# Kernel tuning notes

Hardware: AMD Instinct MI355X
Metric: run time of the kernel (lower is better)

Reference implementation:

```python
import jax, jax.numpy as jnp
import numpy as np
import math

D_MODEL = 1024
NUM_HEADS = 16
D_K = D_MODEL // NUM_HEADS
SEQ = 4096
THETA = 10000.0


def _rope_tables(d_k, max_seq_len, theta):
    freqs = 1.0 / theta ** (jnp.arange(0, d_k, 2, dtype=jnp.float32) / d_k)  # (d_k/2,)
    pos = jnp.arange(max_seq_len, dtype=jnp.float32)
    ang = pos[:, None] * freqs[None, :]  # (S, d_k/2)
    return jnp.cos(ang), jnp.sin(ang)


def setup_inputs() -> dict:
    key = jax.random.key(0)
    ks = jax.random.split(key, 5)
    std = math.sqrt(2.0 / (D_MODEL + D_MODEL))
    def trunc_w(k):
        return jax.random.truncated_normal(k, -3.0, 3.0, (D_MODEL, D_MODEL), jnp.float32) * std
    x = jax.random.normal(ks[0], (1, SEQ, D_MODEL), jnp.float32)
    Wq, Wk, Wv, Wo = trunc_w(ks[1]), trunc_w(ks[2]), trunc_w(ks[3]), trunc_w(ks[4])
    cos, sin = _rope_tables(D_K, SEQ, THETA)
    positions = jnp.arange(SEQ, dtype=jnp.int32)
    return {"x": x, "Wq": Wq, "Wk": Wk, "Wv": Wv, "Wo": Wo,
            "cos": cos, "sin": sin, "positions": positions}


def _apply_rope(t, cos, sin, positions):
    # t: (b, h, s, d_k); cos/sin: (max_s, d_k/2)
    c = cos[positions][None, None]  # (1,1,s,d_k/2)
    s = sin[positions][None, None]
    x1, x2 = t[..., ::2], t[..., 1::2]
    rotated = jnp.stack([x1 * c - x2 * s, x1 * s + x2 * c], axis=-1)  # (b,h,s,d_k/2,2)
    return rotated.reshape(t.shape)


def reference(x, Wq, Wk, Wv, Wo, cos, sin, positions):
    b, s, d = x.shape
    h, dk = NUM_HEADS, D_K
    def proj(W):
        y = jnp.einsum('bsi,oi->bso', x, W)
        return y.reshape(b, s, h, dk).transpose(0, 2, 1, 3)  # (b,h,s,dk)
    Q, K, V = proj(Wq), proj(Wk), proj(Wv)
    Q = _apply_rope(Q, cos, sin, positions)
    K = _apply_rope(K, cos, sin, positions)
    scores = jnp.einsum('bhqd,bhkd->bhqk', Q, K) / math.sqrt(dk)
    causal = jnp.tril(jnp.ones((s, s), dtype=bool))
    scores = jnp.where(causal[None, None], scores, -jnp.inf)
    weights = jax.nn.softmax(scores, axis=-1)
    y = jnp.einsum('bhqk,bhkd->bhqd', weights, V)
    y = y.transpose(0, 2, 1, 3).reshape(b, s, d)
    return jnp.einsum('bsi,oi->bso', y, Wo)
```

## Files before the change

kernel.cpp:

```cpp
#include <hip/hip_runtime.h>
#include <math.h>

#define SEQ 4096
#define DM  1024
#define NH  16
#define DK  64

typedef __attribute__((ext_vector_type(4))) float f32x4;
typedef __attribute__((ext_vector_type(8))) short bf16x8;
typedef __attribute__((ext_vector_type(8))) unsigned short u16x8;

union FragU { u16x8 u; bf16x8 b; ushort4 q[2]; unsigned w[4]; };

__device__ __forceinline__ unsigned cvtpk(float a, float b) {
    unsigned r; asm("v_cvt_pk_bf16_f32 %0, %1, %2" : "=v"(r) : "v"(a), "v"(b)); return r;
}
__device__ __forceinline__ float fexp2(float x) {
    float r; asm("v_exp_f32 %0, %1" : "=v"(r) : "v"(x)); return r;
}
__device__ __forceinline__ float bf_f(unsigned short s) {
    return __uint_as_float(((unsigned)s) << 16);
}
__device__ __forceinline__ void split4(float4 v, ushort4& hv, ushort4& lv) {
    union { ushort4 q; unsigned w[2]; } H, L;
    H.w[0] = cvtpk(v.x, v.y); H.w[1] = cvtpk(v.z, v.w);
    const float rx = v.x - __uint_as_float(H.w[0] << 16);
    const float ry = v.y - __uint_as_float(H.w[0] & 0xffff0000u);
    const float rz = v.z - __uint_as_float(H.w[1] << 16);
    const float rw = v.w - __uint_as_float(H.w[1] & 0xffff0000u);
    L.w[0] = cvtpk(rx, ry); L.w[1] = cvtpk(rz, rw);
    hv = H.q; lv = L.q;
}
__device__ __forceinline__ void split1(float f, unsigned short& h, unsigned short& l) {
    const unsigned hw = cvtpk(f, f) & 0xffffu;
    h = (unsigned short)hw;
    const float r = f - __uint_as_float(hw << 16);
    l = (unsigned short)(__float_as_uint(r) >> 16);
}

template<int MODE>
__global__ __launch_bounds__(256, 2)
void gemm_mfma(const float* __restrict__ Af,
               const unsigned short* __restrict__ Ahi, const unsigned short* __restrict__ Alo,
               const float* __restrict__ W0, const float* __restrict__ W1,
               const float* __restrict__ W2,
               unsigned short* __restrict__ OQh, unsigned short* __restrict__ OQl,
               unsigned short* __restrict__ OKh, unsigned short* __restrict__ OKl,
               unsigned short* __restrict__ OVh,
               float* __restrict__ Ofp,
               const float* __restrict__ cosT, const float* __restrict__ sinT,
               const int* __restrict__ positions)
{
    constexpr int NT = (MODE == 4) ? 24 : 8;
    __shared__ unsigned short As[128][76];
    __shared__ unsigned short Bs[128][76];

    const int t   = threadIdx.x;
    const int bid = blockIdx.x;
    const int qpx = (32 * NT) >> 3;
    const int swz = (bid & 7) * qpx + (bid >> 3);
    const int by  = swz / NT;
    const int bxf = swz % NT;
    const int wt  = (MODE == 4) ? (bxf >> 3) : 0;
    const int bx  = (MODE == 4) ? (bxf & 7) : bxf;
    const int m0  = by * 128;
    const float* W = (MODE == 4) ? (wt == 0 ? W0 : (wt == 1 ? W1 : W2)) : W0;

    const int lane = t & 63, w = t >> 6;
    const int wr = w >> 1, wc = w & 1;
    const int l15 = lane & 15, lg = lane >> 4;

    const int ar = t >> 1, ah = t & 1;
    const float* Ap = (MODE == 4) ? &Af[(size_t)(m0 + ar) * DM + ah * 16] : nullptr;
    const unsigned short* Aph = (MODE == 0) ? &Ahi[(size_t)(m0 + ar) * DM + ah * 16] : nullptr;
    const unsigned short* Apl = (MODE == 0) ? &Alo[(size_t)(m0 + ar) * DM + ah * 16] : nullptr;
    const float* Wp = &W[(size_t)(bx * 128 + ar) * DM + ah * 16];

    f32x4 acc[4][4];
#pragma unroll
    for (int mi = 0; mi < 4; ++mi)
#pragma unroll
        for (int ni = 0; ni < 4; ++ni) acc[mi][ni] = (f32x4){0.f, 0.f, 0.f, 0.f};

    float4 pa[4], pb[4];
    u16x8 pah[2], pal[2];
    if constexpr (MODE == 4) {
#pragma unroll
        for (int g = 0; g < 4; ++g) pa[g] = *reinterpret_cast<const float4*>(Ap + g * 4);
    } else {
        pah[0] = *reinterpret_cast<const u16x8*>(Aph);
        pah[1] = *reinterpret_cast<const u16x8*>(Aph + 8);
        pal[0] = *reinterpret_cast<const u16x8*>(Apl);
        pal[1] = *reinterpret_cast<const u16x8*>(Apl + 8);
    }
#pragma unroll
    for (int g = 0; g < 4; ++g) pb[g] = *reinterpret_cast<const float4*>(Wp + g * 4);

    for (int kt = 0; kt < 32; ++kt) {
        if constexpr (MODE == 4) {
#pragma unroll
            for (int g = 0; g < 4; ++g) {
                ushort4 hv, lv;
                split4(pa[g], hv, lv);
                *reinterpret_cast<ushort4*>(&As[ar][8 * g + 4 * ah])      = hv;
                *reinterpret_cast<ushort4*>(&As[ar][32 + 8 * g + 4 * ah]) = lv;
            }
        } else {
            FragU h0, h1, l0, l1;
            h0.u = pah[0]; h1.u = pah[1]; l0.u = pal[0]; l1.u = pal[1];
            *reinterpret_cast<ushort4*>(&As[ar][0  + 4 * ah]) = h0.q[0];
            *reinterpret_cast<ushort4*>(&As[ar][8  + 4 * ah]) = h0.q[1];
            *reinterpret_cast<ushort4*>(&As[ar][16 + 4 * ah]) = h1.q[0];
            *reinterpret_cast<ushort4*>(&As[ar][24 + 4 * ah]) = h1.q[1];
            *reinterpret_cast<ushort4*>(&As[ar][32 + 4 * ah]) = l0.q[0];
            *reinterpret_cast<ushort4*>(&As[ar][40 + 4 * ah]) = l0.q[1];
            *reinterpret_cast<ushort4*>(&As[ar][48 + 4 * ah]) = l1.q[0];
            *reinterpret_cast<ushort4*>(&As[ar][56 + 4 * ah]) = l1.q[1];
        }
#pragma unroll
        for (int g = 0; g < 4; ++g) {
            ushort4 hv, lv;
            split4(pb[g], hv, lv);
            *reinterpret_cast<ushort4*>(&Bs[ar][8 * g + 4 * ah])      = hv;
            *reinterpret_cast<ushort4*>(&Bs[ar][32 + 8 * g + 4 * ah]) = lv;
        }
        __syncthreads();

        if (kt < 31) {
            const int ko = (kt + 1) * 32;
            if constexpr (MODE == 4) {
#pragma unroll
                for (int g = 0; g < 4; ++g)
                    pa[g] = *reinterpret_cast<const float4*>(Ap + ko + g * 4);
            } else {
                pah[0] = *reinterpret_cast<const u16x8*>(Aph + ko);
                pah[1] = *reinterpret_cast<const u16x8*>(Aph + ko + 8);
                pal[0] = *reinterpret_cast<const u16x8*>(Apl + ko);
                pal[1] = *reinterpret_cast<const u16x8*>(Apl + ko + 8);
            }
#pragma unroll
            for (int g = 0; g < 4; ++g)
                pb[g] = *reinterpret_cast<const float4*>(Wp + ko + g * 4);
        }

        FragU b_h[4], b_l[4];
#pragma unroll
        for (int ni = 0; ni < 4; ++ni) {
            const int row = wc * 64 + ni * 16 + l15;
            b_h[ni].u = *reinterpret_cast<const u16x8*>(&Bs[row][8 * lg]);
            b_l[ni].u = *reinterpret_cast<const u16x8*>(&Bs[row][32 + 8 * lg]);
        }
#pragma unroll
        for (int mi = 0; mi < 4; ++mi) {
            FragU a_h, a_l;
            const int row = wr * 64 + mi * 16 + l15;
            a_h.u = *reinterpret_cast<const u16x8*>(&As[row][8 * lg]);
            a_l.u = *reinterpret_cast<const u16x8*>(&As[row][32 + 8 * lg]);
#pragma unroll
            for (int ni = 0; ni < 4; ++ni) {
                f32x4 c = acc[mi][ni];
                c = __builtin_amdgcn_mfma_f32_16x16x32_bf16(a_h.b, b_h[ni].b, c, 0, 0, 0);
                c = __builtin_amdgcn_mfma_f32_16x16x32_bf16(a_h.b, b_l[ni].b, c, 0, 0, 0);
                c = __builtin_amdgcn_mfma_f32_16x16x32_bf16(a_l.b, b_h[ni].b, c, 0, 0, 0);
                acc[mi][ni] = c;
            }
        }
        __syncthreads();
    }

    if constexpr (MODE == 0) {
#pragma unroll
        for (int mi = 0; mi < 4; ++mi)
#pragma unroll
            for (int ni = 0; ni < 4; ++ni)
#pragma unroll
                for (int r = 0; r < 4; ++r) {
                    const int m = m0 + wr * 64 + mi * 16 + lg * 4 + r;
                    const int n = bx * 128 + wc * 64 + ni * 16 + l15;
                    Ofp[(size_t)m * DM + n] = acc[mi][ni][r];
                }
    } else if (wt == 2) {
#pragma unroll
        for (int mi = 0; mi < 4; ++mi)
#pragma unroll
            for (int ni = 0; ni < 4; ++ni) {
                ushort4 hv;
                unsigned short* hp_ = (unsigned short*)&hv;
#pragma unroll
                for (int r = 0; r < 4; ++r)
                    hp_[r] = (unsigned short)(cvtpk(acc[mi][ni][r], acc[mi][ni][r]) & 0xffffu);
                const int vrow = bx * 128 + wc * 64 + ni * 16 + l15;
                const size_t off = (size_t)vrow * SEQ + m0 + wr * 64 + mi * 16 + lg * 4;
                *reinterpret_cast<ushort4*>(&OVh[off]) = hv;
            }
    } else {
        unsigned short* Oh = (wt == 0) ? OQh : OKh;
        unsigned short* Ol = (wt == 0) ? OQl : OKl;
        const int head = bx * 2 + wc;
        const float qsc = 0.1803368801f;
#pragma unroll
        for (int mi = 0; mi < 4; ++mi)
#pragma unroll
            for (int r = 0; r < 4; ++r) {
                const int m   = m0 + wr * 64 + mi * 16 + lg * 4 + r;
                const int pos = positions[m];
#pragma unroll
                for (int ni = 0; ni < 4; ++ni) {
                    float val = acc[mi][ni][r];
                    const int d = ni * 16 + l15;
                    const float other = __shfl_xor(val, 1);
                    const float cc = cosT[pos * 32 + ni * 8 + (l15 >> 1)];
                    const float ss = sinT[pos * 32 + ni * 8 + (l15 >> 1)];
                    val = (d & 1) ? fmaf(other, ss, val * cc)
                                  : fmaf(other, -ss, val * cc);
                    if (wt == 0) val *= qsc;
                    unsigned short hh, ll;
                    split1(val, hh, ll);
                    const size_t off = ((size_t)head * SEQ + m) * DK + d;
                    Oh[off] = hh; Ol[off] = ll;
                }
            }
    }
}

__global__ __launch_bounds__(256, 2)
void attn_mfma(const unsigned short* __restrict__ Qhi, const unsigned short* __restrict__ Qlo,
               const unsigned short* __restrict__ Khi, const unsigned short* __restrict__ Klo,
               const unsigned short* __restrict__ Vhi,
               unsigned short* __restrict__ Yh, unsigned short* __restrict__ Yl,
               unsigned short* __restrict__ Pb,
               float2* __restrict__ mlA, float2* __restrict__ mlB)
{
    __shared__ unsigned short KsH[64][64], KsL[64][64], Vs[64][64];

    const int t = threadIdx.x, lane = t & 63, w = t >> 6;
    const int bid  = blockIdx.x;
    const int xcd  = bid & 7;
    const int s    = bid >> 3;
    const int hl   = s & 1;
    const int slot = s >> 1;
    const int p    = slot & 15;
    const int half = slot >> 4;
    const int h    = 2 * xcd + hl;

    const int l15 = lane & 15, lg = lane >> 4, dg = lg * 4;
    const int srow = t >> 2, q16 = t & 3;
    const int wh = w & 1;

    int wcol[4];
#pragma unroll
    for (int m = 0; m < 4; ++m) {
        const int g = (q16 >> 1) * 4 + m;
        wcol[m] = (((g ^ (srow & 7)) << 3) + ((q16 & 1) << 2));
    }

    u16x8 pf[6];
    auto PREFETCH = [&](int ktn) {
        const size_t gK = ((size_t)h * SEQ + (size_t)ktn * 64 + srow) * DK + q16 * 16;
        const size_t gV = ((size_t)h * DK + srow) * SEQ + (size_t)ktn * 64 + q16 * 16;
        pf[0] = *reinterpret_cast<const u16x8*>(&Khi[gK]);
        pf[1] = *reinterpret_cast<const u16x8*>(&Khi[gK + 8]);
        pf[2] = *reinterpret_cast<const u16x8*>(&Klo[gK]);
        pf[3] = *reinterpret_cast<const u16x8*>(&Klo[gK + 8]);
        pf[4] = *reinterpret_cast<const u16x8*>(&Vhi[gV]);
        pf[5] = *reinterpret_cast<const u16x8*>(&Vhi[gV + 8]);
    };

    const int nph = (half == 0) ? 2 : 1;
#pragma unroll 1
    for (int ph = 0; ph < nph; ++ph) {
        const int qt    = (half == 0 && ph == 0) ? p : (31 - p);
        const int kt0   = (half == 1) ? (31 - 2 * p) : 0;
        const int kt1   = (half == 0) ? ((ph == 0) ? (2 * p + 2) : (31 - 2 * p))
                                      : (64 - 2 * p);
        const int emode = (half == 0) ? ph : 2;
        const int diagkt = 2 * qt + (w >> 1);

        bf16x8 qh[2][2], ql[2][2];
#pragma unroll
        for (int u = 0; u < 2; ++u) {
            const size_t qrow = ((size_t)h * SEQ + (size_t)qt * 128 + w * 32 + u * 16 + l15) * DK;
#pragma unroll
            for (int c = 0; c < 2; ++c) {
                FragU uh, ul;
                uh.q[0] = *reinterpret_cast<const ushort4*>(&Qhi[qrow + c * 32 + dg]);
                uh.q[1] = *reinterpret_cast<const ushort4*>(&Qhi[qrow + c * 32 + 16 + dg]);
                ul.q[0] = *reinterpret_cast<const ushort4*>(&Qlo[qrow + c * 32 + dg]);
                ul.q[1] = *reinterpret_cast<const ushort4*>(&Qlo[qrow + c * 32 + 16 + dg]);
                qh[u][c] = uh.b; ql[u][c] = ul.b;
            }
        }

        f32x4 yacc[2][4];
#pragma unroll
        for (int u = 0; u < 2; ++u)
#pragma unroll
            for (int dt = 0; dt < 4; ++dt) yacc[u][dt] = (f32x4){0.f, 0.f, 0.f, 0.f};
        float m_run[2] = {-1e30f, -1e30f}, l_run[2] = {0.f, 0.f};

        PREFETCH(kt0);

        for (int kt = kt0; kt < kt1; ++kt) {
            __syncthreads();
            {
                FragU f;
                f.u = pf[0];
                *reinterpret_cast<ushort4*>(&KsH[srow][wcol[0]]) = f.q[0];
                *reinterpret_cast<ushort4*>(&KsH[srow][wcol[1]]) = f.q[1];
                f.u = pf[1];
                *reinterpret_cast<ushort4*>(&KsH[srow][wcol[2]]) = f.q[0];
                *reinterpret_cast<ushort4*>(&KsH[srow][wcol[3]]) = f.q[1];
                f.u = pf[2];
                *reinterpret_cast<ushort4*>(&KsL[srow][wcol[0]]) = f.q[0];
                *reinterpret_cast<ushort4*>(&KsL[srow][wcol[1]]) = f.q[1];
                f.u = pf[3];
                *reinterpret_cast<ushort4*>(&KsL[srow][wcol[2]]) = f.q[0];
                *reinterpret_cast<ushort4*>(&KsL[srow][wcol[3]]) = f.q[1];
                f.u = pf[4];
                *reinterpret_cast<ushort4*>(&Vs[srow][wcol[0]]) = f.q[0];
                *reinterpret_cast<ushort4*>(&Vs[srow][wcol[1]]) = f.q[1];
                f.u = pf[5];
                *reinterpret_cast<ushort4*>(&Vs[srow][wcol[2]]) = f.q[0];
                *reinterpret_cast<ushort4*>(&Vs[srow][wcol[3]]) = f.q[1];
            }
            __syncthreads();

            if (kt + 1 < kt1) PREFETCH(kt + 1);

            if (kt > diagkt) continue;
            const bool diag = (kt == diagkt);

            f32x4 st[2][4];
            __builtin_amdgcn_s_setprio(1);
#pragma unroll
            for (int ktile = 0; ktile < 4; ++ktile) {
                const int rowK = ktile * 16 + l15;
                const int swk  = rowK & 7;
                FragU kh0, kl0, kh1, kl1;
                {
                    const int p0 = ((0 + lg) ^ swk) << 3;
                    const int p1 = ((4 + lg) ^ swk) << 3;
                    kh0.u = *reinterpret_cast<const u16x8*>(&KsH[rowK][p0]);
                    kl0.u = *reinterpret_cast<const u16x8*>(&KsL[rowK][p0]);
                    kh1.u = *reinterpret_cast<const u16x8*>(&KsH[rowK][p1]);
                    kl1.u = *reinterpret_cast<const u16x8*>(&KsL[rowK][p1]);
                }
#pragma unroll
                for (int u = 0; u < 2; ++u) {
                    if (diag && ktile > wh * 2 + u) {
                        st[u][ktile] = (f32x4){-1e30f, -1e30f, -1e30f, -1e30f};
                        continue;
                    }
                    f32x4 s0 = (f32x4){0.f, 0.f, 0.f, 0.f};
                    s0 = __builtin_amdgcn_mfma_f32_16x16x32_bf16(kh0.b, qh[u][0], s0, 0, 0, 0);
                    s0 = __builtin_amdgcn_mfma_f32_16x16x32_bf16(kh0.b, ql[u][0], s0, 0, 0, 0);
                    s0 = __builtin_amdgcn_mfma_f32_16x16x32_bf16(kl0.b, qh[u][0], s0, 0, 0, 0);
                    s0 = __builtin_amdgcn_mfma_f32_16x16x32_bf16(kh1.b, qh[u][1], s0, 0, 0, 0);
                    s0 = __builtin_amdgcn_mfma_f32_16x16x32_bf16(kh1.b, ql[u][1], s0, 0, 0, 0);
                    s0 = __builtin_amdgcn_mfma_f32_16x16x32_bf16(kl1.b, qh[u][1], s0, 0, 0, 0);
                    st[u][ktile] = s0;
                }
            }
            __builtin_amdgcn_s_setprio(0);

            if (diag) {
#pragma unroll
                for (int u = 0; u < 2; ++u) {
                    const int ub = wh * 2 + u;
#pragma unroll
                    for (int r = 0; r < 4; ++r)
                        if (dg + r > l15) st[u][ub][r] = -1e30f;
                }
            }

            bf16x8 pa[2][2];
#pragma unroll
            for (int u = 0; u < 2; ++u) {
                float rowmax = st[u][0][0];
#pragma unroll
                for (int ktile = 0; ktile < 4; ++ktile)
#pragma unroll
                    for (int r = 0; r < 4; ++r) rowmax = fmaxf(rowmax, st[u][ktile][r]);
                rowmax = fmaxf(rowmax, __shfl_xor(rowmax, 16));
                rowmax = fmaxf(rowmax, __shfl_xor(rowmax, 32));
                if (!__all(rowmax <= m_run[u] + 11.5f)) {
                    const float mnew = fmaxf(m_run[u], rowmax);
                    const float factor = fexp2(m_run[u] - mnew);
                    l_run[u] *= factor;
#pragma unroll
                    for (int r = 0; r < 4; ++r) {
                        const float fr = __shfl(factor, (lg << 2) | r);
#pragma unroll
                        for (int dt = 0; dt < 4; ++dt) yacc[u][dt][r] *= fr;
                    }
                    m_run[u] = mnew;
                }
                float pp[4][4]; float psum = 0.f;
#pragma unroll
                for (int ktile = 0; ktile < 4; ++ktile)
#pragma unroll
                    for (int r = 0; r < 4; ++r) {
                        pp[ktile][r] = fexp2(st[u][ktile][r] - m_run[u]);
                        psum += pp[ktile][r];
                    }
                psum += __shfl_xor(psum, 16);
                psum += __shfl_xor(psum, 32);
                l_run[u] += psum;
#pragma unroll
                for (int c = 0; c < 2; ++c) {
                    FragU P;
                    P.w[0] = cvtpk(pp[2 * c][0],     pp[2 * c][1]);
                    P.w[1] = cvtpk(pp[2 * c][2],     pp[2 * c][3]);
                    P.w[2] = cvtpk(pp[2 * c + 1][0], pp[2 * c + 1][1]);
                    P.w[3] = cvtpk(pp[2 * c + 1][2], pp[2 * c + 1][3]);
                    pa[u][c] = P.b;
                }
            }

            __builtin_amdgcn_s_setprio(1);
#pragma unroll
            for (int dt = 0; dt < 4; ++dt) {
                const int rowV = dt * 16 + l15;
                const int swv  = rowV & 7;
#pragma unroll
                for (int c = 0; c < 2; ++c) {
                    FragU vh;
                    vh.u = *reinterpret_cast<const u16x8*>(&Vs[rowV][((c * 4 + lg) ^ swv) << 3]);
#pragma unroll
                    for (int u = 0; u < 2; ++u) {
                        if (diag && c == 1 && (wh * 2 + u) < 2) continue;
                        yacc[u][dt] = __builtin_amdgcn_mfma_f32_16x16x32_bf16(pa[u][c], vh.b, yacc[u][dt], 0, 0, 0);
                    }
                }
            }
            __builtin_amdgcn_s_setprio(0);
        }

        if (emode == 0) {
#pragma unroll
            for (int u = 0; u < 2; ++u) {
                const float inv = 1.0f / l_run[u];
#pragma unroll
                for (int r = 0; r < 4; ++r) {
                    const float ir = __shfl(inv, (lg << 2) | r);
                    const size_t row = (size_t)qt * 128 + w * 32 + u * 16 + lg * 4 + r;
#pragma unroll
                    for (int dt = 0; dt < 4; ++dt) {
                        unsigned short hh, ll;
                        split1(yacc[u][dt][r] * ir, hh, ll);
                        const size_t off = row * DM + h * DK + dt * 16 + l15;
                        Yh[off] = hh; Yl[off] = ll;
                    }
                }
            }
        } else if (emode == 1) {
#pragma unroll
            for (int u = 0; u < 2; ++u) {
#pragma unroll
                for (int r = 0; r < 4; ++r) {
                    const size_t row = (size_t)qt * 128 + w * 32 + u * 16 + lg * 4 + r;
#pragma unroll
                    for (int dt = 0; dt < 4; ++dt) {
                        unsigned short hh, ll;
                        split1(yacc[u][dt][r], hh, ll);
                        const size_t off = row * DM + h * DK + dt * 16 + l15;
                        Yh[off] = hh; Yl[off] = ll;
                    }
                }
                if (lane < 16)
                    mlA[(h * 16 + p) * 128 + w * 32 + u * 16 + lane] =
                        make_float2(m_run[u], l_run[u]);
            }
        } else {
#pragma unroll
            for (int u = 0; u < 2; ++u) {
#pragma unroll
                for (int r = 0; r < 4; ++r) {
                    const int rloc = w * 32 + u * 16 + lg * 4 + r;
#pragma unroll
                    for (int dt = 0; dt < 4; ++dt) {
                        Pb[((size_t)(h * 16 + p) * 128 + rloc) * 64 + dt * 16 + l15] =
                            (unsigned short)(cvtpk(yacc[u][dt][r], yacc[u][dt][r]) & 0xffffu);
                    }
                }
                if (lane < 16)
                    mlB[(h * 16 + p) * 128 + w * 32 + u * 16 + lane] =
                        make_float2(m_run[u], l_run[u]);
            }
        }
    }
}

__global__ __launch_bounds__(256)
void merge_heavy(unsigned short* __restrict__ Yh, unsigned short* __restrict__ Yl,
                 const unsigned short* __restrict__ Pb,
                 const float2* __restrict__ mlA, const float2* __restrict__ mlB)
{
    const int hp = blockIdx.x;
    const int h = hp >> 4, p = hp & 15;
    const int t = threadIdx.x;
    const int row = t >> 1;
    const int d0 = (t & 1) * 32;
    const float2 a = mlA[hp * 128 + row];
    const float2 b = mlB[hp * 128 + row];
    const float m  = fmaxf(a.x, b.x);
    const float fA = fexp2(a.x - m), fB = fexp2(b.x - m);
    const float inv = 1.0f / (fA * a.y + fB * b.y);
    const size_t rg = ((size_t)(31 - p) * 128 + row) * DM + h * DK + d0;
    const size_t pg = ((size_t)hp * 128 + row) * 64 + d0;
#pragma unroll
    for (int dd = 0; dd < 32; dd += 8) {
        u16x8 vh = *reinterpret_cast<const u16x8*>(&Yh[rg + dd]);
        u16x8 vl = *reinterpret_cast<const u16x8*>(&Yl[rg + dd]);
        u16x8 vb = *reinterpret_cast<const u16x8*>(&Pb[pg + dd]);
        u16x8 oh, ol;
#pragma unroll
        for (int j = 0; j < 8; ++j) {
            const float ya = bf_f(vh[j]) + bf_f(vl[j]);
            const float yb = bf_f(vb[j]);
            const float o  = (fA * ya + fB * yb) * inv;
            unsigned short hh, ll;
            split1(o, hh, ll);
            oh[j] = hh; ol[j] = ll;
        }
        *reinterpret_cast<u16x8*>(&Yh[rg + dd]) = oh;
        *reinterpret_cast<u16x8*>(&Yl[rg + dd]) = ol;
    }
}

extern "C" void kernel_launch(void* const* d_in, const int* in_sizes, int n_in,
                              void* d_out, int out_size, void* d_ws, size_t ws_size,
                              hipStream_t stream)
{
    const float* x    = (const float*)d_in[0];
    const float* Wq   = (const float*)d_in[1];
    const float* Wk   = (const float*)d_in[2];
    const float* Wv   = (const float*)d_in[3];
    const float* Wo   = (const float*)d_in[4];
    const float* cosT = (const float*)d_in[5];
    const float* sinT = (const float*)d_in[6];
    const int*   pos  = (const int*)d_in[7];
    float* out = (float*)d_out;

    const size_t E = (size_t)SEQ * DM;
    unsigned short* qh = (unsigned short*)d_ws;
    unsigned short* ql = qh + E;
    unsigned short* kh = ql + E;
    unsigned short* kl = kh + E;
    unsigned short* vh = kl + E;
    unsigned short* yh = vh + E;
    unsigned short* yl = yh + E;
    unsigned short* Pb = yl + E;
    float2* mlA = (float2*)(Pb + (size_t)256 * 128 * 64);
    float2* mlB = mlA + (size_t)256 * 128;

    gemm_mfma<4><<<dim3(768), dim3(256), 0, stream>>>(
        x, nullptr, nullptr, Wq, Wk, Wv,
        qh, ql, kh, kl, vh, nullptr, cosT, sinT, pos);
    attn_mfma<<<dim3(512), dim3(256), 0, stream>>>(
        qh, ql, kh, kl, vh, yh, yl, Pb, mlA, mlB);
    merge_heavy<<<dim3(256), dim3(256), 0, stream>>>(yh, yl, Pb, mlA, mlB);
    gemm_mfma<0><<<dim3(256), dim3(256), 0, stream>>>(
        nullptr, yh, yl, Wo, nullptr, nullptr,
        nullptr, nullptr, nullptr, nullptr, nullptr, out, cosT, sinT, pos);
}
```

Measured before the change: 273.2 us.

## Pre-split x into bf16 hi/lo and double-buffer K/V tiles in attention

A new kernel splits x into bf16 hi/lo halves once, so the QKV GEMM reads pre-split A operands instead of redoing the split in each of the 24 column blocks. The attention kernel now double-buffers its K/V shared-memory tiles, removing one barrier per iteration and overlapping staging of the next tile with compute. It also drops the s_setprio hints. The cost is an extra kernel launch, an extra pass over x in memory, and twice the LDS use in attention. The workspace is reshuffled so the Y buffers reuse the x split buffers.

```diff
diff --git a/kernel.cpp b/kernel.cpp
--- a/kernel.cpp
+++ b/kernel.cpp
@@ -38,10 +38,23 @@
     l = (unsigned short)(__float_as_uint(r) >> 16);
 }
 
+__global__ __launch_bounds__(256)
+void split_f32(const float* __restrict__ src, unsigned short* __restrict__ hi,
+               unsigned short* __restrict__ lo, int n4)
+{
+    const int stride = gridDim.x * 256;
+    for (int i = blockIdx.x * 256 + threadIdx.x; i < n4; i += stride) {
+        const float4 v = reinterpret_cast<const float4*>(src)[i];
+        ushort4 hv, lv;
+        split4(v, hv, lv);
+        reinterpret_cast<ushort4*>(hi)[i] = hv;
+        reinterpret_cast<ushort4*>(lo)[i] = lv;
+    }
+}
+
 template<int MODE>
 __global__ __launch_bounds__(256, 2)
-void gemm_mfma(const float* __restrict__ Af,
-               const unsigned short* __restrict__ Ahi, const unsigned short* __restrict__ Alo,
+void gemm_mfma(const unsigned short* __restrict__ Ahi, const unsigned short* __restrict__ Alo,
                const float* __restrict__ W0, const float* __restrict__ W1,
                const float* __restrict__ W2,
                unsigned short* __restrict__ OQh, unsigned short* __restrict__ OQl,
@@ -71,9 +84,8 @@
     const int l15 = lane & 15, lg = lane >> 4;
 
     const int ar = t >> 1, ah = t & 1;
-    const float* Ap = (MODE == 4) ? &Af[(size_t)(m0 + ar) * DM + ah * 16] : nullptr;
-    const unsigned short* Aph = (MODE == 0) ? &Ahi[(size_t)(m0 + ar) * DM + ah * 16] : nullptr;
-    const unsigned short* Apl = (MODE == 0) ? &Alo[(size_t)(m0 + ar) * DM + ah * 16] : nullptr;
+    const unsigned short* Aph = &Ahi[(size_t)(m0 + ar) * DM + ah * 16];
+    const unsigned short* Apl = &Alo[(size_t)(m0 + ar) * DM + ah * 16];
     const float* Wp = &W[(size_t)(bx * 128 + ar) * DM + ah * 16];
 
     f32x4 acc[4][4];
@@ -82,30 +94,17 @@
 #pragma unroll
         for (int ni = 0; ni < 4; ++ni) acc[mi][ni] = (f32x4){0.f, 0.f, 0.f, 0.f};
 
-    float4 pa[4], pb[4];
+    float4 pb[4];
     u16x8 pah[2], pal[2];
-    if constexpr (MODE == 4) {
-#pragma unroll
-        for (int g = 0; g < 4; ++g) pa[g] = *reinterpret_cast<const float4*>(Ap + g * 4);
-    } else {
-        pah[0] = *reinterpret_cast<const u16x8*>(Aph);
-        pah[1] = *reinterpret_cast<const u16x8*>(Aph + 8);
-        pal[0] = *reinterpret_cast<const u16x8*>(Apl);
-        pal[1] = *reinterpret_cast<const u16x8*>(Apl + 8);
-    }
+    pah[0] = *reinterpret_cast<const u16x8*>(Aph);
+    pah[1] = *reinterpret_cast<const u16x8*>(Aph + 8);
+    pal[0] = *reinterpret_cast<const u16x8*>(Apl);
+    pal[1] = *reinterpret_cast<const u16x8*>(Apl + 8);
 #pragma unroll
     for (int g = 0; g < 4; ++g) pb[g] = *reinterpret_cast<const float4*>(Wp + g * 4);
 
     for (int kt = 0; kt < 32; ++kt) {
-        if constexpr (MODE == 4) {
-#pragma unroll
-            for (int g = 0; g < 4; ++g) {
-                ushort4 hv, lv;
-                split4(pa[g], hv, lv);
-                *reinterpret_cast<ushort4*>(&As[ar][8 * g + 4 * ah])      = hv;
-                *reinterpret_cast<ushort4*>(&As[ar][32 + 8 * g + 4 * ah]) = lv;
-            }
-        } else {
+        {
             FragU h0, h1, l0, l1;
             h0.u = pah[0]; h1.u = pah[1]; l0.u = pal[0]; l1.u = pal[1];
             *reinterpret_cast<ushort4*>(&As[ar][0  + 4 * ah]) = h0.q[0];
@@ -128,16 +127,10 @@
 
         if (kt < 31) {
             const int ko = (kt + 1) * 32;
-            if constexpr (MODE == 4) {
-#pragma unroll
-                for (int g = 0; g < 4; ++g)
-                    pa[g] = *reinterpret_cast<const float4*>(Ap + ko + g * 4);
-            } else {
-                pah[0] = *reinterpret_cast<const u16x8*>(Aph + ko);
-                pah[1] = *reinterpret_cast<const u16x8*>(Aph + ko + 8);
-                pal[0] = *reinterpret_cast<const u16x8*>(Apl + ko);
-                pal[1] = *reinterpret_cast<const u16x8*>(Apl + ko + 8);
-            }
+            pah[0] = *reinterpret_cast<const u16x8*>(Aph + ko);
+            pah[1] = *reinterpret_cast<const u16x8*>(Aph + ko + 8);
+            pal[0] = *reinterpret_cast<const u16x8*>(Apl + ko);
+            pal[1] = *reinterpret_cast<const u16x8*>(Apl + ko + 8);
 #pragma unroll
             for (int g = 0; g < 4; ++g)
                 pb[g] = *reinterpret_cast<const float4*>(Wp + ko + g * 4);
@@ -231,7 +224,7 @@
                unsigned short* __restrict__ Pb,
                float2* __restrict__ mlA, float2* __restrict__ mlB)
 {
-    __shared__ unsigned short KsH[64][64], KsL[64][64], Vs[64][64];
+    __shared__ unsigned short KsH[2][64][64], KsL[2][64][64], Vs[2][64][64];
 
     const int t = threadIdx.x, lane = t & 63, w = t >> 6;
     const int bid  = blockIdx.x;
@@ -265,6 +258,27 @@
         pf[4] = *reinterpret_cast<const u16x8*>(&Vhi[gV]);
         pf[5] = *reinterpret_cast<const u16x8*>(&Vhi[gV + 8]);
     };
+    auto STAGE = [&](int b) {
+        FragU f;
+        f.u = pf[0];
+        *reinterpret_cast<ushort4*>(&KsH[b][srow][wcol[0]]) = f.q[0];
+        *reinterpret_cast<ushort4*>(&KsH[b][srow][wcol[1]]) = f.q[1];
+        f.u = pf[1];
+        *reinterpret_cast<ushort4*>(&KsH[b][srow][wcol[2]]) = f.q[0];
+        *reinterpret_cast<ushort4*>(&KsH[b][srow][wcol[3]]) = f.q[1];
+        f.u = pf[2];
+        *reinterpret_cast<ushort4*>(&KsL[b][srow][wcol[0]]) = f.q[0];
+        *reinterpret_cast<ushort4*>(&KsL[b][srow][wcol[1]]) = f.q[1];
+        f.u = pf[3];
+        *reinterpret_cast<ushort4*>(&KsL[b][srow][wcol[2]]) = f.q[0];
+        *reinterpret_cast<ushort4*>(&KsL[b][srow][wcol[3]]) = f.q[1];
+        f.u = pf[4];
+        *reinterpret_cast<ushort4*>(&Vs[b][srow][wcol[0]]) = f.q[0];
+        *reinterpret_cast<ushort4*>(&Vs[b][srow][wcol[1]]) = f.q[1];
+        f.u = pf[5];
+        *reinterpret_cast<ushort4*>(&Vs[b][srow][wcol[2]]) = f.q[0];
+        *reinterpret_cast<ushort4*>(&Vs[b][srow][wcol[3]]) = f.q[1];
+    };
 
     const int nph = (half == 0) ? 2 : 1;
 #pragma unroll 1
@@ -299,141 +313,122 @@
         float m_run[2] = {-1e30f, -1e30f}, l_run[2] = {0.f, 0.f};
 
         PREFETCH(kt0);
+        __syncthreads();
+        STAGE(0);
+        if (kt0 + 1 < kt1) PREFETCH(kt0 + 1);
 
         for (int kt = kt0; kt < kt1; ++kt) {
+            const int b = (kt - kt0) & 1;
             __syncthreads();
-            {
-                FragU f;
-                f.u = pf[0];
-                *reinterpret_cast<ushort4*>(&KsH[srow][wcol[0]]) = f.q[0];
-                *reinterpret_cast<ushort4*>(&KsH[srow][wcol[1]]) = f.q[1];
-                f.u = pf[1];
-                *reinterpret_cast<ushort4*>(&KsH[srow][wcol[2]]) = f.q[0];
-                *reinterpret_cast<ushort4*>(&KsH[srow][wcol[3]]) = f.q[1];
-                f.u = pf[2];
-                *reinterpret_cast<ushort4*>(&KsL[srow][wcol[0]]) = f.q[0];
-                *reinterpret_cast<ushort4*>(&KsL[srow][wcol[1]]) = f.q[1];
-                f.u = pf[3];
-                *reinterpret_cast<ushort4*>(&KsL[srow][wcol[2]]) = f.q[0];
-                *reinterpret_cast<ushort4*>(&KsL[srow][wcol[3]]) = f.q[1];
-                f.u = pf[4];
-                *reinterpret_cast<ushort4*>(&Vs[srow][wcol[0]]) = f.q[0];
-                *reinterpret_cast<ushort4*>(&Vs[srow][wcol[1]]) = f.q[1];
-                f.u = pf[5];
-                *reinterpret_cast<ushort4*>(&Vs[srow][wcol[2]]) = f.q[0];
-                *reinterpret_cast<ushort4*>(&Vs[srow][wcol[3]]) = f.q[1];
-            }
-            __syncthreads();
-
-            if (kt + 1 < kt1) PREFETCH(kt + 1);
-
-            if (kt > diagkt) continue;
-            const bool diag = (kt == diagkt);
-
-            f32x4 st[2][4];
-            __builtin_amdgcn_s_setprio(1);
-#pragma unroll
-            for (int ktile = 0; ktile < 4; ++ktile) {
-                const int rowK = ktile * 16 + l15;
-                const int swk  = rowK & 7;
-                FragU kh0, kl0, kh1, kl1;
-                {
-                    const int p0 = ((0 + lg) ^ swk) << 3;
-                    const int p1 = ((4 + lg) ^ swk) << 3;
-                    kh0.u = *reinterpret_cast<const u16x8*>(&KsH[rowK][p0]);
-                    kl0.u = *reinterpret_cast<const u16x8*>(&KsL[rowK][p0]);
-                    kh1.u = *reinterpret_cast<const u16x8*>(&KsH[rowK][p1]);
-                    kl1.u = *reinterpret_cast<const u16x8*>(&KsL[rowK][p1]);
-                }
+            if (kt + 1 < kt1) {
+                STAGE(b ^ 1);
+                if (kt + 2 < kt1) PREFETCH(kt + 2);
+            }
+
+            if (kt <= diagkt) {
+                const bool diag = (kt == diagkt);
+
+                f32x4 st[2][4];
+#pragma unroll
+                for (int ktile = 0; ktile < 4; ++ktile) {
+                    const int rowK = ktile * 16 + l15;
+                    const int swk  = rowK & 7;
+                    FragU kh0, kl0, kh1, kl1;
+                    {
+                        const int p0 = ((0 + lg) ^ swk) << 3;
+                        const int p1 = ((4 + lg) ^ swk) << 3;
+                        kh0.u = *reinterpret_cast<const u16x8*>(&KsH[b][rowK][p0]);
+                        kl0.u = *reinterpret_cast<const u16x8*>(&KsL[b][rowK][p0]);
+                        kh1.u = *reinterpret_cast<const u16x8*>(&KsH[b][rowK][p1]);
+                        kl1.u = *reinterpret_cast<const u16x8*>(&KsL[b][rowK][p1]);
+                    }
+#pragma unroll
+                    for (int u = 0; u < 2; ++u) {
+                        if (diag && ktile > wh * 2 + u) {
+                            st[u][ktile] = (f32x4){-1e30f, -1e30f, -1e30f, -1e30f};
+                            continue;
+                        }
+                        f32x4 s0 = (f32x4){0.f, 0.f, 0.f, 0.f};
+                        s0 = __builtin_amdgcn_mfma_f32_16x16x32_bf16(kh0.b, qh[u][0], s0, 0, 0, 0);
+                        s0 = __builtin_amdgcn_mfma_f32_16x16x32_bf16(kh0.b, ql[u][0], s0, 0, 0, 0);
+                        s0 = __builtin_amdgcn_mfma_f32_16x16x32_bf16(kl0.b, qh[u][0], s0, 0, 0, 0);
+                        s0 = __builtin_amdgcn_mfma_f32_16x16x32_bf16(kh1.b, qh[u][1], s0, 0, 0, 0);
+                        s0 = __builtin_amdgcn_mfma_f32_16x16x32_bf16(kh1.b, ql[u][1], s0, 0, 0, 0);
+                        s0 = __builtin_amdgcn_mfma_f32_16x16x32_bf16(kl1.b, qh[u][1], s0, 0, 0, 0);
+                        st[u][ktile] = s0;
+                    }
+                }
+
+                if (diag) {
+#pragma unroll
+                    for (int u = 0; u < 2; ++u) {
+                        const int ub = wh * 2 + u;
+#pragma unroll
+                        for (int r = 0; r < 4; ++r)
+                            if (dg + r > l15) st[u][ub][r] = -1e30f;
+                    }
+                }
+
+                bf16x8 pa[2][2];
 #pragma unroll
                 for (int u = 0; u < 2; ++u) {
-                    if (diag && ktile > wh * 2 + u) {
-                        st[u][ktile] = (f32x4){-1e30f, -1e30f, -1e30f, -1e30f};
-                        continue;
-                    }
-                    f32x4 s0 = (f32x4){0.f, 0.f, 0.f, 0.f};
-                    s0 = __builtin_amdgcn_mfma_f32_16x16x32_bf16(kh0.b, qh[u][0], s0, 0, 0, 0);
-                    s0 = __builtin_amdgcn_mfma_f32_16x16x32_bf16(kh0.b, ql[u][0], s0, 0, 0, 0);
-                    s0 = __builtin_amdgcn_mfma_f32_16x16x32_bf16(kl0.b, qh[u][0], s0, 0, 0, 0);
-                    s0 = __builtin_amdgcn_mfma_f32_16x16x32_bf16(kh1.b, qh[u][1], s0, 0, 0, 0);
-                    s0 = __builtin_amdgcn_mfma_f32_16x16x32_bf16(kh1.b, ql[u][1], s0, 0, 0, 0);
-                    s0 = __builtin_amdgcn_mfma_f32_16x16x32_bf16(kl1.b, qh[u][1], s0, 0, 0, 0);
-                    st[u][ktile] = s0;
-                }
-            }
-            __builtin_amdgcn_s_setprio(0);
-
-            if (diag) {
-#pragma unroll
-                for (int u = 0; u < 2; ++u) {
-                    const int ub = wh * 2 + u;
-#pragma unroll
-                    for (int r = 0; r < 4; ++r)
-                        if (dg + r > l15) st[u][ub][r] = -1e30f;
-                }
-            }
-
-            bf16x8 pa[2][2];
-#pragma unroll
-            for (int u = 0; u < 2; ++u) {
-                float rowmax = st[u][0][0];
-#pragma unroll
-                for (int ktile = 0; ktile < 4; ++ktile)
-#pragma unroll
-                    for (int r = 0; r < 4; ++r) rowmax = fmaxf(rowmax, st[u][ktile][r]);
-                rowmax = fmaxf(rowmax, __shfl_xor(rowmax, 16));
-                rowmax = fmaxf(rowmax, __shfl_xor(rowmax, 32));
-                if (!__all(rowmax <= m_run[u] + 11.5f)) {
-                    const float mnew = fmaxf(m_run[u], rowmax);
-                    const float factor = fexp2(m_run[u] - mnew);
-                    l_run[u] *= factor;
-#pragma unroll
-                    for (int r = 0; r < 4; ++r) {
-                        const float fr = __shfl(factor, (lg << 2) | r);
-#pragma unroll
-                        for (int dt = 0; dt < 4; ++dt) yacc[u][dt][r] *= fr;
-                    }
-                    m_run[u] = mnew;
-                }
-                float pp[4][4]; float psum = 0.f;
-#pragma unroll
-                for (int ktile = 0; ktile < 4; ++ktile)
-#pragma unroll
-                    for (int r = 0; r < 4; ++r) {
-                        pp[ktile][r] = fexp2(st[u][ktile][r] - m_run[u]);
-                        psum += pp[ktile][r];
-                    }
-                psum += __shfl_xor(psum, 16);
-                psum += __shfl_xor(psum, 32);
-                l_run[u] += psum;
-#pragma unroll
-                for (int c = 0; c < 2; ++c) {
-                    FragU P;
-                    P.w[0] = cvtpk(pp[2 * c][0],     pp[2 * c][1]);
-                    P.w[1] = cvtpk(pp[2 * c][2],     pp[2 * c][3]);
-                    P.w[2] = cvtpk(pp[2 * c + 1][0], pp[2 * c + 1][1]);
-                    P.w[3] = cvtpk(pp[2 * c + 1][2], pp[2 * c + 1][3]);
-                    pa[u][c] = P.b;
-                }
-            }
-
-            __builtin_amdgcn_s_setprio(1);
-#pragma unroll
-            for (int dt = 0; dt < 4; ++dt) {
-                const int rowV = dt * 16 + l15;
-                const int swv  = rowV & 7;
-#pragma unroll
-                for (int c = 0; c < 2; ++c) {
-                    FragU vh;
-                    vh.u = *reinterpret_cast<const u16x8*>(&Vs[rowV][((c * 4 + lg) ^ swv) << 3]);
-#pragma unroll
-                    for (int u = 0; u < 2; ++u) {
-                        if (diag && c == 1 && (wh * 2 + u) < 2) continue;
-                        yacc[u][dt] = __builtin_amdgcn_mfma_f32_16x16x32_bf16(pa[u][c], vh.b, yacc[u][dt], 0, 0, 0);
-                    }
-                }
-            }
-            __builtin_amdgcn_s_setprio(0);
+                    float rowmax = st[u][0][0];
+#pragma unroll
+                    for (int ktile = 0; ktile < 4; ++ktile)
+#pragma unroll
+                        for (int r = 0; r < 4; ++r) rowmax = fmaxf(rowmax, st[u][ktile][r]);
+                    rowmax = fmaxf(rowmax, __shfl_xor(rowmax, 16));
+                    rowmax = fmaxf(rowmax, __shfl_xor(rowmax, 32));
+                    if (!__all(rowmax <= m_run[u] + 11.5f)) {
+                        const float mnew = fmaxf(m_run[u], rowmax);
+                        const float factor = fexp2(m_run[u] - mnew);
+                        l_run[u] *= factor;
+#pragma unroll
+                        for (int r = 0; r < 4; ++r) {
+                            const float fr = __shfl(factor, (lg << 2) | r);
+#pragma unroll
+                            for (int dt = 0; dt < 4; ++dt) yacc[u][dt][r] *= fr;
+                        }
+                        m_run[u] = mnew;
+                    }
+                    float pp[4][4]; float psum = 0.f;
+#pragma unroll
+                    for (int ktile = 0; ktile < 4; ++ktile)
+#pragma unroll
+                        for (int r = 0; r < 4; ++r) {
+                            pp[ktile][r] = fexp2(st[u][ktile][r] - m_run[u]);
+                            psum += pp[ktile][r];
+                        }
+                    psum += __shfl_xor(psum, 16);
+                    psum += __shfl_xor(psum, 32);
+                    l_run[u] += psum;
+#pragma unroll
+                    for (int c = 0; c < 2; ++c) {
+                        FragU P;
+                        P.w[0] = cvtpk(pp[2 * c][0],     pp[2 * c][1]);
+                        P.w[1] = cvtpk(pp[2 * c][2],     pp[2 * c][3]);
+                        P.w[2] = cvtpk(pp[2 * c + 1][0], pp[2 * c + 1][1]);
+                        P.w[3] = cvtpk(pp[2 * c + 1][2], pp[2 * c + 1][3]);
+                        pa[u][c] = P.b;
+                    }
+                }
+
+#pragma unroll
+                for (int dt = 0; dt < 4; ++dt) {
+                    const int rowV = dt * 16 + l15;
+                    const int swv  = rowV & 7;
+#pragma unroll
+                    for (int c = 0; c < 2; ++c) {
+                        FragU vh;
+                        vh.u = *reinterpret_cast<const u16x8*>(&Vs[b][rowV][((c * 4 + lg) ^ swv) << 3]);
+#pragma unroll
+                        for (int u = 0; u < 2; ++u) {
+                            if (diag && c == 1 && (wh * 2 + u) < 2) continue;
+                            yacc[u][dt] = __builtin_amdgcn_mfma_f32_16x16x32_bf16(pa[u][c], vh.b, yacc[u][dt], 0, 0, 0);
+                        }
+                    }
+                }
+            }
         }
 
         if (emode == 0) {
@@ -543,24 +538,26 @@
     float* out = (float*)d_out;
 
     const size_t E = (size_t)SEQ * DM;
-    unsigned short* qh = (unsigned short*)d_ws;
+    unsigned short* xh = (unsigned short*)d_ws;
+    unsigned short* xl = xh + E;
+    unsigned short* qh = xl + E;
     unsigned short* ql = qh + E;
     unsigned short* kh = ql + E;
     unsigned short* kl = kh + E;
     unsigned short* vh = kl + E;
-    unsigned short* yh = vh + E;
-    unsigned short* yl = yh + E;
-    unsigned short* Pb = yl + E;
+    unsigned short* Pb = vh + E;
     float2* mlA = (float2*)(Pb + (size_t)256 * 128 * 64);
     float2* mlB = mlA + (size_t)256 * 128;
-
+    unsigned short* yh = xh;
+    unsigned short* yl = xl;
+
+    split_f32<<<dim3(1024), dim3(256), 0, stream>>>(x, xh, xl, (int)(E / 4));
     gemm_mfma<4><<<dim3(768), dim3(256), 0, stream>>>(
-        x, nullptr, nullptr, Wq, Wk, Wv,
-        qh, ql, kh, kl, vh, nullptr, cosT, sinT, pos);
+        xh, xl, Wq, Wk, Wv, qh, ql, kh, kl, vh, nullptr, cosT, sinT, pos);
     attn_mfma<<<dim3(512), dim3(256), 0, stream>>>(
         qh, ql, kh, kl, vh, yh, yl, Pb, mlA, mlB);
     merge_heavy<<<dim3(256), dim3(256), 0, stream>>>(yh, yl, Pb, mlA, mlB);
     gemm_mfma<0><<<dim3(256), dim3(256), 0, stream>>>(
-        nullptr, yh, yl, Wo, nullptr, nullptr,
+        yh, yl, Wo, nullptr, nullptr,
         nullptr, nullptr, nullptr, nullptr, nullptr, out, cosT, sinT, pos);
 }
```

Result: no change. 275.9 us (+1.0%).
